# Performance work log

Hardware: AMD Instinct MI355X
Metric: run time of the kernel (lower is better)

## Reference

```python
import jax, jax.numpy as jnp
import numpy as np

NEG_SLOPE = 0.2  # PyG GATConv default LeakyReLU slope


def gat_layer(x, src, dst, W, a_src, a_dst, bias, heads, out_dim, concat, n_nodes):
    # x: [N, F_in]; W: [F_in, heads*out_dim]
    h = (x @ W).reshape(n_nodes, heads, out_dim)          # [N, H, C]
    alpha_src = jnp.sum(h * a_src, axis=-1)               # [N, H]
    alpha_dst = jnp.sum(h * a_dst, axis=-1)               # [N, H]
    e = jax.nn.leaky_relu(alpha_src[src] + alpha_dst[dst], NEG_SLOPE)  # [E, H]
    # softmax over edges grouped by destination node (self-loops guarantee nonempty segments)
    m = jax.ops.segment_max(e, dst, num_segments=n_nodes)  # [N, H]
    w = jnp.exp(e - m[dst])
    s = jax.ops.segment_sum(w, dst, num_segments=n_nodes)  # [N, H]
    alpha = w / s[dst]                                     # [E, H]
    msg = h[src] * alpha[:, :, None]                       # [E, H, C]
    out = jax.ops.segment_sum(msg, dst, num_segments=n_nodes)  # [N, H, C]
    if concat:
        out = out.reshape(n_nodes, heads * out_dim)
    else:
        out = out.mean(axis=1)
    return out + bias


def setup_inputs() -> dict:
    key = jax.random.key(0)
    ks = jax.random.split(key, 12)
    N, E = 50000, 600000
    F_IN, OUT = 256, 64
    H1, C1 = 2, 2 * OUT          # conv1: heads=2, per-head dim 128
    F2 = H1 * C1                 # 256
    x = jax.random.normal(ks[0], (N, F_IN), dtype=jnp.float32)
    edge_index = jax.random.randint(ks[1], (2, E), 0, N, dtype=jnp.int64)
    g1 = 1.0 / np.sqrt(F_IN)
    g2 = 1.0 / np.sqrt(F2)
    return {
        "x": x,
        "edge_index": edge_index,
        "W1": jax.random.normal(ks[2], (F_IN, H1 * C1), dtype=jnp.float32) * g1,
        "a1_src": jax.random.normal(ks[3], (H1, C1), dtype=jnp.float32) * g2,
        "a1_dst": jax.random.normal(ks[4], (H1, C1), dtype=jnp.float32) * g2,
        "b1": jnp.zeros((H1 * C1,), dtype=jnp.float32),
        "W2": jax.random.normal(ks[5], (F2, OUT), dtype=jnp.float32) * g2,
        "a2_src": jax.random.normal(ks[6], (1, OUT), dtype=jnp.float32) * 0.1,
        "a2_dst": jax.random.normal(ks[7], (1, OUT), dtype=jnp.float32) * 0.1,
        "b2": jnp.zeros((OUT,), dtype=jnp.float32),
    }


def reference(x, edge_index, W1, a1_src, a1_dst, b1, W2, a2_src, a2_dst, b2):
    N = x.shape[0]
    # add self-loops (PyG GATConv default)
    loops = jnp.arange(N, dtype=edge_index.dtype)
    src = jnp.concatenate([edge_index[0], loops])
    dst = jnp.concatenate([edge_index[1], loops])
    OUT = W2.shape[1]
    h = gat_layer(x, src, dst, W1, a1_src, a1_dst, b1,
                  heads=2, out_dim=2 * OUT, concat=True, n_nodes=N)
    h = jax.nn.elu(h)
    out = gat_layer(h, src, dst, W2, a2_src, a2_dst, b2,
                    heads=1, out_dim=OUT, concat=False, n_nodes=N)
    return out
```

## Files before the change

### kernel.cpp

```cpp
#include <hip/hip_runtime.h>
#include <hip/hip_bf16.h>
#include <math.h>


#define NSLOPE 0.2f

using bf16x8 = __attribute__((ext_vector_type(8))) short;
using f32x4  = __attribute__((ext_vector_type(4))) float;
using u16x8  = __attribute__((ext_vector_type(8))) unsigned short;
using u16x4  = __attribute__((ext_vector_type(4))) unsigned short;

__device__ __forceinline__ unsigned short bf16_rne(float f) {
    unsigned u = __float_as_uint(f);
    return (unsigned short)((u + 0x7FFFu + ((u >> 16) & 1u)) >> 16);
}
__device__ __forceinline__ float bf16_to_f(unsigned short h) {
    return __uint_as_float(((unsigned)h) << 16);
}

__global__ __launch_bounds__(256) void k_prep_all(const float* __restrict__ x,
                                                  const float* __restrict__ W1,
                                                  const float* __restrict__ W2,
                                                  const int* __restrict__ edst,
                                                  unsigned short* __restrict__ Xhi,
                                                  unsigned short* __restrict__ W1hi,
                                                  unsigned short* __restrict__ W1lo,
                                                  unsigned short* __restrict__ W2hi,
                                                  int* __restrict__ deg,
                                                  int BX, int total4, int E) {
    int b = blockIdx.x, t = threadIdx.x;
    if (b < BX) {
        int id = b * 256 + t;
        if (id >= total4) return;
        float4 v = *(const float4*)&x[(size_t)id * 4];
        unsigned short hi[4];
        hi[0] = bf16_rne(v.x); hi[1] = bf16_rne(v.y);
        hi[2] = bf16_rne(v.z); hi[3] = bf16_rne(v.w);
        *(u16x4*)&Xhi[(size_t)id * 4] = *(u16x4*)hi;
    } else if (b < BX + 64) {
        int id = (b - BX) * 256 + t;
        int n = id >> 6, kg = id & 63;
        unsigned short hi[4], lo[4];
#pragma unroll
        for (int c = 0; c < 4; ++c) {
            float w = W1[(kg * 4 + c) * 256 + n];
            unsigned short h = bf16_rne(w);
            hi[c] = h;
            lo[c] = bf16_rne(w - bf16_to_f(h));
        }
        *(u16x4*)&W1hi[n * 256 + kg * 4] = *(u16x4*)hi;
        *(u16x4*)&W1lo[n * 256 + kg * 4] = *(u16x4*)lo;
    } else if (b < BX + 128) {
        int id = (b - BX - 64) * 256 + t;
        int n = id >> 8, k = id & 255;
        W2hi[n * 256 + k] = bf16_rne(W2[k * 64 + n]);
    } else {
        int i = (b - BX - 128) * 256 + t;
        if (i < E) atomicAdd(&deg[edst[i]], 1);
    }
}

__global__ __launch_bounds__(256) void k_scan_ab(const int* __restrict__ deg,
                                                 int* __restrict__ part,
                                                 int* __restrict__ ticket,
                                                 int* __restrict__ off_n,
                                                 int n, int CH) {
    __shared__ int sd[256];
    __shared__ int lastflag;
    int b = blockIdx.x, t = threadIdx.x;
    int s = b * CH, e = min(n, s + CH);
    int loc = 0;
    for (int i = s + t; i < e; i += 256) loc += deg[i] + 1;
    sd[t] = loc;
    __syncthreads();
    for (int o = 128; o > 0; o >>= 1) {
        if (t < o) sd[t] += sd[t + o];
        __syncthreads();
    }
    if (t == 0) {
        part[b] = sd[0];
        __threadfence();
        int old = atomicAdd(ticket, 1);
        lastflag = (old == (int)gridDim.x - 1);
    }
    __syncthreads();
    if (lastflag) {
        __threadfence();
        int v = ((volatile int*)part)[t];
        sd[t] = v;
        __syncthreads();
        for (int o = 1; o < 256; o <<= 1) {
            int u = (t >= o) ? sd[t - o] : 0;
            __syncthreads();
            sd[t] += u;
            __syncthreads();
        }
        part[t] = sd[t] - v;
        if (t == 255) *off_n = sd[255];
    }
}

__global__ __launch_bounds__(256) void k_scan_c(const int* __restrict__ deg,
                                                const int* __restrict__ part,
                                                int* __restrict__ off,
                                                int* __restrict__ cur,
                                                int* __restrict__ srcl, int n, int CH) {
    __shared__ int sd[256];
    int b = blockIdx.x, t = threadIdx.x;
    int s = b * CH, e = min(n, s + CH);
    int base = part[b];
    for (int c = s; c < e; c += 256) {
        int i = c + t;
        int v = (i < e) ? (deg[i] + 1) : 0;
        sd[t] = v;
        __syncthreads();
        for (int o = 1; o < 256; o <<= 1) {
            int u = (t >= o) ? sd[t - o] : 0;
            __syncthreads();
            sd[t] += u;
            __syncthreads();
        }
        if (i < e) {
            int ex = base + sd[t] - v;
            off[i] = ex;
            cur[i] = ex + 1;
            srcl[ex] = i;
        }
        base += sd[255];
        __syncthreads();
    }
}

__global__ void k_fill(const int* __restrict__ src, const int* __restrict__ dst,
                       int* cur, int* __restrict__ srcl, int E) {
    int i = blockIdx.x * blockDim.x + threadIdx.x;
    if (i >= E) return;
    int s = src[i], d = dst[i];
    int p = atomicAdd(&cur[d], 1);
    srcl[p] = s;
}

#define G1S 40
__global__ __launch_bounds__(256) void k_gemm1(const unsigned short* __restrict__ Xhi,
                                               const unsigned short* __restrict__ Whi,
                                               const unsigned short* __restrict__ Wlo,
                                               const float* __restrict__ a1s,
                                               const float* __restrict__ a1d,
                                               unsigned short* __restrict__ h1b,
                                               float* __restrict__ as_,
                                               float* __restrict__ ad_, int M) {
    __shared__ unsigned short sAh[128 * G1S];
    __shared__ unsigned short sBh[128 * G1S], sBl[128 * G1S];
    __shared__ float salS[128][2], salD[128][2];
    int t = threadIdx.x;
    int lane = t & 63, wave = t >> 6;
    int q = lane >> 4, m = lane & 15;
    int row0 = blockIdx.x * 128;
    int head = blockIdx.y;
    int col0 = head * 128;
    int rbase = (wave & 1) * 64, cbase = (wave >> 1) * 64;
    f32x4 acc[4][4];
#pragma unroll
    for (int i = 0; i < 4; ++i)
#pragma unroll
        for (int j = 0; j < 4; ++j) acc[i][j] = (f32x4){0.f, 0.f, 0.f, 0.f};

    for (int kc = 0; kc < 256; kc += 32) {
#pragma unroll
        for (int i2 = 0; i2 < 2; ++i2) {
            int slot = t + i2 * 256;
            int r = slot >> 2, kg = slot & 3;
            int row = row0 + r;
            u16x8 vh = {0, 0, 0, 0, 0, 0, 0, 0};
            if (row < M) vh = *(const u16x8*)&Xhi[(size_t)row * 256 + kc + kg * 8];
            *(u16x8*)&sAh[r * G1S + kg * 8] = vh;
        }
#pragma unroll
        for (int i2 = 0; i2 < 2; ++i2) {
            int slot = t + i2 * 256;
            int n = slot >> 2, kg = slot & 3;
            *(u16x8*)&sBh[n * G1S + kg * 8] =
                *(const u16x8*)&Whi[(size_t)(col0 + n) * 256 + kc + kg * 8];
            *(u16x8*)&sBl[n * G1S + kg * 8] =
                *(const u16x8*)&Wlo[(size_t)(col0 + n) * 256 + kc + kg * 8];
        }
        __syncthreads();
        bf16x8 ah[4], bh[4], bl[4];
#pragma unroll
        for (int i = 0; i < 4; ++i)
            ah[i] = *(bf16x8*)&sAh[(rbase + i * 16 + m) * G1S + q * 8];
#pragma unroll
        for (int j = 0; j < 4; ++j) {
            int r = (cbase + j * 16 + m) * G1S + q * 8;
            bh[j] = *(bf16x8*)&sBh[r];
            bl[j] = *(bf16x8*)&sBl[r];
        }
#pragma unroll
        for (int i = 0; i < 4; ++i)
#pragma unroll
            for (int j = 0; j < 4; ++j) {
                acc[i][j] = __builtin_amdgcn_mfma_f32_16x16x32_bf16(ah[i], bl[j], acc[i][j], 0, 0, 0);
                acc[i][j] = __builtin_amdgcn_mfma_f32_16x16x32_bf16(ah[i], bh[j], acc[i][j], 0, 0, 0);
            }
        __syncthreads();
    }
    float sv[4], dv[4];
#pragma unroll
    for (int j = 0; j < 4; ++j) {
        sv[j] = a1s[head * 128 + cbase + j * 16 + m];
        dv[j] = a1d[head * 128 + cbase + j * 16 + m];
    }
#pragma unroll
    for (int i = 0; i < 4; ++i) {
#pragma unroll
        for (int r = 0; r < 4; ++r) {
            int rl = rbase + i * 16 + q * 4 + r;
            int row = row0 + rl;
            float ps = acc[i][0][r] * sv[0] + acc[i][1][r] * sv[1]
                     + acc[i][2][r] * sv[2] + acc[i][3][r] * sv[3];
            float pd = acc[i][0][r] * dv[0] + acc[i][1][r] * dv[1]
                     + acc[i][2][r] * dv[2] + acc[i][3][r] * dv[3];
#pragma unroll
            for (int mask = 1; mask < 16; mask <<= 1) {
                ps += __shfl_xor(ps, mask, 64);
                pd += __shfl_xor(pd, mask, 64);
            }
            if (m == 0) {
                salS[rl][cbase >> 6] = ps;
                salD[rl][cbase >> 6] = pd;
            }
            if (row < M) {
#pragma unroll
                for (int j = 0; j < 4; ++j)
                    h1b[(size_t)row * 256 + col0 + cbase + j * 16 + m] = bf16_rne(acc[i][j][r]);
            }
        }
    }
    __syncthreads();
    if (t < 128) {
        int row = row0 + t;
        if (row < M) {
            as_[row * 2 + head] = salS[t][0] + salS[t][1];
            ad_[row * 2 + head] = salD[t][0] + salD[t][1];
        }
    }
}

__global__ __launch_bounds__(256) void k_agg1(const unsigned short* __restrict__ h1b,
                                              const float* __restrict__ as,
                                              const float* __restrict__ ad,
                                              const int* __restrict__ off,
                                              const int* __restrict__ srcl,
                                              const float* __restrict__ b1,
                                              unsigned short* __restrict__ helu_b, int N) {
    int wid = (blockIdx.x * blockDim.x + threadIdx.x) >> 6;
    int lane = threadIdx.x & 63;
    if (wid >= N) return;
    int p0 = off[wid], p1 = off[wid + 1];
    float ad0 = ad[wid * 2], ad1 = ad[wid * 2 + 1];
    int half = lane >> 5, hl = lane & 31;
    int headL = hl >> 4;
    float acc[8];
#pragma unroll
    for (int c = 0; c < 8; ++c) acc[c] = 0.f;
    float sumw = 0.f;
    for (int base = p0; base < p1; base += 64) {
        int p = base + lane;
        int cnt = min(64, p1 - base);
        int s = 0; float w0 = 0.f, w1 = 0.f;
        if (p < p1) {
            s = srcl[p];
            float2 av = *(const float2*)&as[s * 2];
            float l0 = av.x + ad0; l0 = l0 >= 0.f ? l0 : NSLOPE * l0;
            float l1 = av.y + ad1; l1 = l1 >= 0.f ? l1 : NSLOPE * l1;
            w0 = __expf(l0); w1 = __expf(l1);
        }
        int pairs = (cnt + 1) >> 1;
        int jj = 0;
        for (; jj + 2 <= pairs; jj += 2) {
            int e0 = 2 * jj + half, e1 = e0 + 2;
            int sa = __shfl(s, e0, 64), sb = __shfl(s, e1, 64);
            float wa0 = __shfl(w0, e0, 64), wa1 = __shfl(w1, e0, 64);
            float wb0 = __shfl(w0, e1, 64), wb1 = __shfl(w1, e1, 64);
            u16x8 hva = *(const u16x8*)&h1b[(size_t)sa * 256 + hl * 8];
            u16x8 hvb = *(const u16x8*)&h1b[(size_t)sb * 256 + hl * 8];
            float wa = headL ? wa1 : wa0;
            float wb = headL ? wb1 : wb0;
            sumw += wa + wb;
#pragma unroll
            for (int c = 0; c < 8; ++c)
                acc[c] += wa * bf16_to_f(hva[c]) + wb * bf16_to_f(hvb[c]);
        }
        for (; jj < pairs; ++jj) {
            int e0 = 2 * jj + half;
            int sa = __shfl(s, e0, 64);
            float wa0 = __shfl(w0, e0, 64), wa1 = __shfl(w1, e0, 64);
            u16x8 hva = *(const u16x8*)&h1b[(size_t)sa * 256 + hl * 8];
            float wa = headL ? wa1 : wa0;
            sumw += wa;
#pragma unroll
            for (int c = 0; c < 8; ++c) acc[c] += wa * bf16_to_f(hva[c]);
        }
    }
#pragma unroll
    for (int c = 0; c < 8; ++c) acc[c] += __shfl_xor(acc[c], 32, 64);
    sumw += __shfl_xor(sumw, 32, 64);
    float inv = 1.0f / sumw;
    int ch = hl * 8 + half * 4;
    float4 bv = *(const float4*)&b1[ch];
    float bb[4] = {bv.x, bv.y, bv.z, bv.w};
    unsigned short o[4];
#pragma unroll
    for (int c = 0; c < 4; ++c) {
        float v = acc[half * 4 + c] * inv + bb[c];
        v = v > 0.f ? v : expm1f(v);
        o[c] = bf16_rne(v);
    }
    *(u16x4*)&helu_b[(size_t)wid * 256 + ch] = *(u16x4*)o;
}

__global__ __launch_bounds__(256) void k_gemm2(const unsigned short* __restrict__ hb,
                                               const unsigned short* __restrict__ Whi,
                                               const float* __restrict__ a2s,
                                               const float* __restrict__ a2d,
                                               unsigned short* __restrict__ h2b,
                                               float* __restrict__ as_,
                                               float* __restrict__ ad_, int M) {
    __shared__ unsigned short sA[128 * G1S];
    __shared__ unsigned short sBh[64 * G1S];
    int t = threadIdx.x;
    int lane = t & 63, wave = t >> 6;
    int q = lane >> 4, m = lane & 15;
    int row0 = blockIdx.x * 128;
    int rbase = wave * 32;
    f32x4 acc[2][4];
#pragma unroll
    for (int i = 0; i < 2; ++i)
#pragma unroll
        for (int j = 0; j < 4; ++j) acc[i][j] = (f32x4){0.f, 0.f, 0.f, 0.f};

    for (int kc = 0; kc < 256; kc += 32) {
#pragma unroll
        for (int i = 0; i < 2; ++i) {
            int slot = t + i * 256;
            int r = slot >> 2, kg = slot & 3;
            int row = row0 + r;
            u16x8 v = {0, 0, 0, 0, 0, 0, 0, 0};
            if (row < M) v = *(const u16x8*)&hb[(size_t)row * 256 + kc + kg * 8];
            *(u16x8*)&sA[r * G1S + kg * 8] = v;
        }
        {
            int n = t >> 2, kg = t & 3;
            *(u16x8*)&sBh[n * G1S + kg * 8] =
                *(const u16x8*)&Whi[(size_t)n * 256 + kc + kg * 8];
        }
        __syncthreads();
        bf16x8 a[2], bh[4];
#pragma unroll
        for (int i = 0; i < 2; ++i)
            a[i] = *(bf16x8*)&sA[(rbase + i * 16 + m) * G1S + q * 8];
#pragma unroll
        for (int j = 0; j < 4; ++j)
            bh[j] = *(bf16x8*)&sBh[(j * 16 + m) * G1S + q * 8];
#pragma unroll
        for (int i = 0; i < 2; ++i)
#pragma unroll
            for (int j = 0; j < 4; ++j)
                acc[i][j] = __builtin_amdgcn_mfma_f32_16x16x32_bf16(a[i], bh[j], acc[i][j], 0, 0, 0);
        __syncthreads();
    }
    float sv[4], dv[4];
#pragma unroll
    for (int j = 0; j < 4; ++j) {
        sv[j] = a2s[j * 16 + m];
        dv[j] = a2d[j * 16 + m];
    }
#pragma unroll
    for (int i = 0; i < 2; ++i) {
#pragma unroll
        for (int r = 0; r < 4; ++r) {
            int row = row0 + rbase + i * 16 + q * 4 + r;
            float ps = acc[i][0][r] * sv[0] + acc[i][1][r] * sv[1]
                     + acc[i][2][r] * sv[2] + acc[i][3][r] * sv[3];
            float pd = acc[i][0][r] * dv[0] + acc[i][1][r] * dv[1]
                     + acc[i][2][r] * dv[2] + acc[i][3][r] * dv[3];
#pragma unroll
            for (int mask = 1; mask < 16; mask <<= 1) {
                ps += __shfl_xor(ps, mask, 64);
                pd += __shfl_xor(pd, mask, 64);
            }
            if (row < M) {
#pragma unroll
                for (int j = 0; j < 4; ++j)
                    h2b[(size_t)row * 64 + j * 16 + m] = bf16_rne(acc[i][j][r]);
                if (m == 0) { as_[row] = ps; ad_[row] = pd; }
            }
        }
    }
}

__global__ __launch_bounds__(256) void k_agg2(const unsigned short* __restrict__ h2b,
                                              const float* __restrict__ as,
                                              const float* __restrict__ ad,
                                              const int* __restrict__ off,
                                              const int* __restrict__ srcl,
                                              const float* __restrict__ b2,
                                              float* __restrict__ out, int N) {
    int wid = (blockIdx.x * blockDim.x + threadIdx.x) >> 6;
    int lane = threadIdx.x & 63;
    if (wid >= N) return;
    int p0 = off[wid], p1 = off[wid + 1];
    float adw = ad[wid];
    int g = lane >> 4, gl = lane & 15;
    float acc[4];
#pragma unroll
    for (int c = 0; c < 4; ++c) acc[c] = 0.f;
    float sumw = 0.f;
    for (int base = p0; base < p1; base += 64) {
        int p = base + lane;
        int cnt = min(64, p1 - base);
        int s = 0; float w = 0.f;
        if (p < p1) {
            s = srcl[p];
            float l = as[s] + adw;
            l = l >= 0.f ? l : NSLOPE * l;
            w = __expf(l);
        }
        int quads = (cnt + 3) >> 2;
        int jj = 0;
        for (; jj + 2 <= quads; jj += 2) {
            int e0 = 4 * jj + g, e1 = e0 + 4;
            int sa = __shfl(s, e0, 64), sb = __shfl(s, e1, 64);
            float wa = __shfl(w, e0, 64), wb = __shfl(w, e1, 64);
            u16x4 hva = *(const u16x4*)&h2b[(size_t)sa * 64 + gl * 4];
            u16x4 hvb = *(const u16x4*)&h2b[(size_t)sb * 64 + gl * 4];
            sumw += wa + wb;
            acc[0] += wa * bf16_to_f(hva.x) + wb * bf16_to_f(hvb.x);
            acc[1] += wa * bf16_to_f(hva.y) + wb * bf16_to_f(hvb.y);
            acc[2] += wa * bf16_to_f(hva.z) + wb * bf16_to_f(hvb.z);
            acc[3] += wa * bf16_to_f(hva.w) + wb * bf16_to_f(hvb.w);
        }
        for (; jj < quads; ++jj) {
            int e0 = 4 * jj + g;
            int sa = __shfl(s, e0, 64);
            float wa = __shfl(w, e0, 64);
            u16x4 hva = *(const u16x4*)&h2b[(size_t)sa * 64 + gl * 4];
            sumw += wa;
            acc[0] += wa * bf16_to_f(hva.x);
            acc[1] += wa * bf16_to_f(hva.y);
            acc[2] += wa * bf16_to_f(hva.z);
            acc[3] += wa * bf16_to_f(hva.w);
        }
    }
#pragma unroll
    for (int c = 0; c < 4; ++c) {
        acc[c] += __shfl_xor(acc[c], 16, 64);
        acc[c] += __shfl_xor(acc[c], 32, 64);
    }
    sumw += __shfl_xor(sumw, 16, 64);
    sumw += __shfl_xor(sumw, 32, 64);
    if (g == 0) {
        float inv = 1.0f / sumw;
        float4 bv = *(const float4*)&b2[gl * 4];
        float4 o;
        o.x = acc[0] * inv + bv.x;
        o.y = acc[1] * inv + bv.y;
        o.z = acc[2] * inv + bv.z;
        o.w = acc[3] * inv + bv.w;
        *(float4*)&out[(size_t)wid * 64 + gl * 4] = o;
    }
}

extern "C" void kernel_launch(void* const* d_in, const int* in_sizes, int n_in,
                              void* d_out, int out_size, void* d_ws, size_t ws_size,
                              hipStream_t stream) {
    if (n_in < 10) return;
    const float* x   = (const float*)d_in[0];
    const int*   ei  = (const int*)d_in[1];
    const float* W1  = (const float*)d_in[2];
    const float* a1s = (const float*)d_in[3];
    const float* a1d = (const float*)d_in[4];
    const float* b1  = (const float*)d_in[5];
    const float* W2  = (const float*)d_in[6];
    const float* a2s = (const float*)d_in[7];
    const float* a2d = (const float*)d_in[8];
    const float* b2  = (const float*)d_in[9];
    float* out = (float*)d_out;

    const int N = in_sizes[0] / 256;
    const int E = in_sizes[1] / 2;
    const int T = E + N;
    const int* esrc = ei;
    const int* edst = ei + E;

    char* ws = (char*)d_ws;
    size_t o = 0;
    auto alloc = [&](size_t bytes) -> void* {
        void* p = ws + o;
        o = (o + bytes + 255) & ~(size_t)255;
        return p;
    };
    size_t szX = (size_t)N * 256 * 2;
    char* regionA = (char*)alloc(szX);
    unsigned short* Xhi    = (unsigned short*)regionA;
    unsigned short* helu_b = (unsigned short*)regionA;

    unsigned short* h1b  = (unsigned short*)alloc((size_t)N * 256 * 2);
    unsigned short* W1hi = (unsigned short*)alloc(256 * 256 * 2);
    unsigned short* W1lo = (unsigned short*)alloc(256 * 256 * 2);
    unsigned short* W2hi = (unsigned short*)alloc(64 * 256 * 2);
    unsigned short* h2b  = (unsigned short*)alloc((size_t)N * 64 * 2);
    float* al1s = (float*)alloc((size_t)N * 2 * 4);
    float* al1d = (float*)alloc((size_t)N * 2 * 4);
    float* al2s = (float*)alloc((size_t)N * 4);
    float* al2d = (float*)alloc((size_t)N * 4);
    int* deg  = (int*)alloc((size_t)(N + 64) * 4);
    int* ticket = deg + N;
    int* off  = (int*)alloc((size_t)(N + 1) * 4);
    int* cur  = (int*)alloc((size_t)N * 4);
    int* part = (int*)alloc(256 * 4);
    int* srcl = (int*)alloc((size_t)T * 4);
    if (o > ws_size) return;

    const int CH = (N + 255) / 256;
    const int total4 = N * 64;
    const int BX = (total4 + 255) / 256;
    const int BH = (E + 255) / 256;

    hipMemsetAsync(deg, 0, (size_t)(N + 64) * 4, stream);
    k_prep_all<<<BX + 128 + BH, 256, 0, stream>>>(x, W1, W2, edst, Xhi,
                                                  W1hi, W1lo, W2hi, deg,
                                                  BX, total4, E);
    k_scan_ab<<<256, 256, 0, stream>>>(deg, part, ticket, &off[N], N, CH);
    k_scan_c<<<256, 256, 0, stream>>>(deg, part, off, cur, srcl, N, CH);
    k_fill<<<(E + 255) / 256, 256, 0, stream>>>(esrc, edst, cur, srcl, E);

    dim3 g1((N + 127) / 128, 2);
    k_gemm1<<<g1, 256, 0, stream>>>(Xhi, W1hi, W1lo, a1s, a1d, h1b, al1s, al1d, N);
    k_agg1<<<(N + 3) / 4, 256, 0, stream>>>(h1b, al1s, al1d, off, srcl, b1, helu_b, N);

    k_gemm2<<<(N + 127) / 128, 256, 0, stream>>>(helu_b, W2hi, a2s, a2d,
                                                 h2b, al2s, al2d, N);
    k_agg2<<<(N + 3) / 4, 256, 0, stream>>>(h2b, al2s, al2d, off, srcl, b2, out, N);
}
```

Baseline: 292.7 us.

## Load GEMM B operand directly from global and widen K chunk to 64

```diff
diff --git a/kernel.cpp b/kernel.cpp
--- a/kernel.cpp
+++ b/kernel.cpp
@@ -140,7 +140,7 @@
     srcl[p] = s;
 }
 
-#define G1S 40
+#define AS 72
 __global__ __launch_bounds__(256) void k_gemm1(const unsigned short* __restrict__ Xhi,
                                                const unsigned short* __restrict__ Whi,
                                                const unsigned short* __restrict__ Wlo,
@@ -149,8 +149,7 @@
                                                unsigned short* __restrict__ h1b,
                                                float* __restrict__ as_,
                                                float* __restrict__ ad_, int M) {
-    __shared__ unsigned short sAh[128 * G1S];
-    __shared__ unsigned short sBh[128 * G1S], sBl[128 * G1S];
+    __shared__ unsigned short sAh[128 * AS];
     __shared__ float salS[128][2], salD[128][2];
     int t = threadIdx.x;
     int lane = t & 63, wave = t >> 6;
@@ -165,43 +164,38 @@
 #pragma unroll
         for (int j = 0; j < 4; ++j) acc[i][j] = (f32x4){0.f, 0.f, 0.f, 0.f};
 
-    for (int kc = 0; kc < 256; kc += 32) {
-#pragma unroll
-        for (int i2 = 0; i2 < 2; ++i2) {
+    const unsigned short* Bh0 = Whi + (size_t)(col0 + cbase + m) * 256;
+    const unsigned short* Bl0 = Wlo + (size_t)(col0 + cbase + m) * 256;
+
+    for (int kc = 0; kc < 256; kc += 64) {
+#pragma unroll
+        for (int i2 = 0; i2 < 4; ++i2) {
             int slot = t + i2 * 256;
-            int r = slot >> 2, kg = slot & 3;
+            int r = slot >> 3, kg = slot & 7;
             int row = row0 + r;
             u16x8 vh = {0, 0, 0, 0, 0, 0, 0, 0};
             if (row < M) vh = *(const u16x8*)&Xhi[(size_t)row * 256 + kc + kg * 8];
-            *(u16x8*)&sAh[r * G1S + kg * 8] = vh;
-        }
-#pragma unroll
-        for (int i2 = 0; i2 < 2; ++i2) {
-            int slot = t + i2 * 256;
-            int n = slot >> 2, kg = slot & 3;
-            *(u16x8*)&sBh[n * G1S + kg * 8] =
-                *(const u16x8*)&Whi[(size_t)(col0 + n) * 256 + kc + kg * 8];
-            *(u16x8*)&sBl[n * G1S + kg * 8] =
-                *(const u16x8*)&Wlo[(size_t)(col0 + n) * 256 + kc + kg * 8];
-        }
-        __syncthreads();
-        bf16x8 ah[4], bh[4], bl[4];
-#pragma unroll
-        for (int i = 0; i < 4; ++i)
-            ah[i] = *(bf16x8*)&sAh[(rbase + i * 16 + m) * G1S + q * 8];
-#pragma unroll
-        for (int j = 0; j < 4; ++j) {
-            int r = (cbase + j * 16 + m) * G1S + q * 8;
-            bh[j] = *(bf16x8*)&sBh[r];
-            bl[j] = *(bf16x8*)&sBl[r];
-        }
-#pragma unroll
-        for (int i = 0; i < 4; ++i)
+            *(u16x8*)&sAh[r * AS + kg * 8] = vh;
+        }
+        __syncthreads();
+#pragma unroll
+        for (int k2 = 0; k2 < 2; ++k2) {
+            int kq = k2 * 32 + q * 8;
+            bf16x8 ah[4];
+#pragma unroll
+            for (int i = 0; i < 4; ++i)
+                ah[i] = *(bf16x8*)&sAh[(rbase + i * 16 + m) * AS + kq];
 #pragma unroll
             for (int j = 0; j < 4; ++j) {
-                acc[i][j] = __builtin_amdgcn_mfma_f32_16x16x32_bf16(ah[i], bl[j], acc[i][j], 0, 0, 0);
-                acc[i][j] = __builtin_amdgcn_mfma_f32_16x16x32_bf16(ah[i], bh[j], acc[i][j], 0, 0, 0);
-            }
+                bf16x8 bh = *(const bf16x8*)&Bh0[(size_t)j * 16 * 256 + kc + kq];
+                bf16x8 bl = *(const bf16x8*)&Bl0[(size_t)j * 16 * 256 + kc + kq];
+#pragma unroll
+                for (int i = 0; i < 4; ++i) {
+                    acc[i][j] = __builtin_amdgcn_mfma_f32_16x16x32_bf16(ah[i], bl, acc[i][j], 0, 0, 0);
+                    acc[i][j] = __builtin_amdgcn_mfma_f32_16x16x32_bf16(ah[i], bh, acc[i][j], 0, 0, 0);
+                }
+            }
+        }
         __syncthreads();
     }
     float sv[4], dv[4];
@@ -326,8 +320,7 @@
                                                unsigned short* __restrict__ h2b,
                                                float* __restrict__ as_,
                                                float* __restrict__ ad_, int M) {
-    __shared__ unsigned short sA[128 * G1S];
-    __shared__ unsigned short sBh[64 * G1S];
+    __shared__ unsigned short sA[128 * AS];
     int t = threadIdx.x;
     int lane = t & 63, wave = t >> 6;
     int q = lane >> 4, m = lane & 15;
@@ -339,34 +332,34 @@
 #pragma unroll
         for (int j = 0; j < 4; ++j) acc[i][j] = (f32x4){0.f, 0.f, 0.f, 0.f};
 
-    for (int kc = 0; kc < 256; kc += 32) {
-#pragma unroll
-        for (int i = 0; i < 2; ++i) {
-            int slot = t + i * 256;
-            int r = slot >> 2, kg = slot & 3;
+    const unsigned short* B0 = Whi + (size_t)m * 256;
+
+    for (int kc = 0; kc < 256; kc += 64) {
+#pragma unroll
+        for (int i2 = 0; i2 < 4; ++i2) {
+            int slot = t + i2 * 256;
+            int r = slot >> 3, kg = slot & 7;
             int row = row0 + r;
             u16x8 v = {0, 0, 0, 0, 0, 0, 0, 0};
             if (row < M) v = *(const u16x8*)&hb[(size_t)row * 256 + kc + kg * 8];
-            *(u16x8*)&sA[r * G1S + kg * 8] = v;
-        }
-        {
-            int n = t >> 2, kg = t & 3;
-            *(u16x8*)&sBh[n * G1S + kg * 8] =
-                *(const u16x8*)&Whi[(size_t)n * 256 + kc + kg * 8];
-        }
-        __syncthreads();
-        bf16x8 a[2], bh[4];
-#pragma unroll
-        for (int i = 0; i < 2; ++i)
-            a[i] = *(bf16x8*)&sA[(rbase + i * 16 + m) * G1S + q * 8];
-#pragma unroll
-        for (int j = 0; j < 4; ++j)
-            bh[j] = *(bf16x8*)&sBh[(j * 16 + m) * G1S + q * 8];
-#pragma unroll
-        for (int i = 0; i < 2; ++i)
-#pragma unroll
-            for (int j = 0; j < 4; ++j)
-                acc[i][j] = __builtin_amdgcn_mfma_f32_16x16x32_bf16(a[i], bh[j], acc[i][j], 0, 0, 0);
+            *(u16x8*)&sA[r * AS + kg * 8] = v;
+        }
+        __syncthreads();
+#pragma unroll
+        for (int k2 = 0; k2 < 2; ++k2) {
+            int kq = k2 * 32 + q * 8;
+            bf16x8 a[2];
+#pragma unroll
+            for (int i = 0; i < 2; ++i)
+                a[i] = *(bf16x8*)&sA[(rbase + i * 16 + m) * AS + kq];
+#pragma unroll
+            for (int j = 0; j < 4; ++j) {
+                bf16x8 bh = *(const bf16x8*)&B0[(size_t)j * 16 * 256 + kc + kq];
+#pragma unroll
+                for (int i = 0; i < 2; ++i)
+                    acc[i][j] = __builtin_amdgcn_mfma_f32_16x16x32_bf16(a[i], bh, acc[i][j], 0, 0, 0);
+            }
+        }
         __syncthreads();
     }
     float sv[4], dv[4];
```

New measurement: 315.9 us. 1.08x slower.
